# Kernel tuning notes

Hardware: AMD Instinct MI355X
Metric: run time of the kernel (lower is better)

The kernel has to match this reference:

```python
import jax, jax.numpy as jnp
import numpy as np

E, H, BLOCK = 1024, 64, 2048

def setup_inputs() -> dict:
    key = jax.random.key(0)
    kx, kk, kq, kv = jax.random.split(key, 4)
    s = 1.0 / np.sqrt(E)
    return {
        "x": jax.random.normal(kx, (16, 2048, E), dtype=jnp.float32),
        "Wk": jax.random.uniform(kk, (E, H), jnp.float32, -s, s),
        "Wq": jax.random.uniform(kq, (E, H), jnp.float32, -s, s),
        "Wv": jax.random.uniform(kv, (E, H), jnp.float32, -s, s),
    }

def reference(x, Wk, Wq, Wv):
    B, T, C = x.shape
    k = x @ Wk  # [B,T,H]
    q = x @ Wq
    v = x @ Wv
    scale = jnp.asarray(H, x.dtype) ** -0.5
    wei = jnp.einsum("bth,bsh->bts", q, k) * scale  # [B,T,T]
    causal = jnp.tril(jnp.ones((T, T), dtype=bool))
    wei = jnp.where(causal, wei, -jnp.inf)
    wei = jax.nn.softmax(wei, axis=-1)
    # dropout is identity in eval mode
    return jnp.einsum("bts,bsh->bth", wei, v)
```

## Files before the change

### kernel.cpp

```cpp
#include <hip/hip_runtime.h>


typedef __bf16 bf16x8 __attribute__((ext_vector_type(8)));
typedef __bf16 bf16x4 __attribute__((ext_vector_type(4)));
typedef float f32x4 __attribute__((ext_vector_type(4)));

constexpr int kE = 1024;
constexpr int kH = 64;
constexpr int kT = 2048;
constexpr int kB = 16;
constexpr int kM = kB * kT;
constexpr float kQScale = 0.125f * 1.44269504088896340736f;

#define MFMA16(a, b, c) __builtin_amdgcn_mfma_f32_16x16x32_bf16((a), (b), (c), 0, 0, 0)

__device__ __forceinline__ void gl_lds16(const void* g, void* l) {
    __builtin_amdgcn_global_load_lds(
        (const __attribute__((address_space(1))) void*)g,
        (__attribute__((address_space(3))) void*)l, 16, 0, 0);
}

__global__ __launch_bounds__(256)
void prep_w(const float* __restrict__ Wq, const float* __restrict__ Wk,
            const float* __restrict__ Wv, __bf16* __restrict__ WbT)
{
    __shared__ float tl[64][65];
    const int mat = blockIdx.x >> 4;
    const int k0 = (blockIdx.x & 15) * 64;
    const float* src = (mat == 0) ? Wq : (mat == 1) ? Wk : Wv;

    const int t = threadIdx.x;
    const int kr = t >> 2;
    const int cg = (t & 3) * 16;
    #pragma unroll
    for (int i = 0; i < 4; ++i) {
        float4 v = *(const float4*)&src[(size_t)(k0 + kr) * kH + cg + 4 * i];
        tl[cg + 4 * i + 0][kr] = v.x;
        tl[cg + 4 * i + 1][kr] = v.y;
        tl[cg + 4 * i + 2][kr] = v.z;
        tl[cg + 4 * i + 3][kr] = v.w;
    }
    __syncthreads();
    const int nl = t >> 2;
    const int kg = (t & 3) * 16;
    bf16x8 o0, o1;
    #pragma unroll
    for (int j = 0; j < 8; ++j) {
        o0[j] = (__bf16)tl[nl][kg + j];
        o1[j] = (__bf16)tl[nl][kg + 8 + j];
    }
    *(bf16x8*)&WbT[(size_t)(mat * 64 + nl) * kE + k0 + kg] = o0;
    *(bf16x8*)&WbT[(size_t)(mat * 64 + nl) * kE + k0 + kg + 8] = o1;
}

__global__ __launch_bounds__(256)
void qkv(const float* __restrict__ x, const __bf16* __restrict__ WbT,
         __bf16* __restrict__ qo, __bf16* __restrict__ ko, __bf16* __restrict__ vT)
{
    __shared__ __align__(16) char Ab[2][16384];
    __shared__ __align__(16) char Bb[2][24576];

    const int t = threadIdx.x;
    const int lane = t & 63;
    const int w = t >> 6;
    const int l15 = lane & 15;
    const int Q = lane >> 4;
    const int row0 = blockIdx.x * 64;

    f32x4 acc[4][3];
    #pragma unroll
    for (int mt = 0; mt < 4; ++mt)
        #pragma unroll
        for (int nt = 0; nt < 3; ++nt) acc[mt][nt] = (f32x4){0.f, 0.f, 0.f, 0.f};

    auto stage = [&](int p, int k0) {
        #pragma unroll
        for (int i = 0; i < 4; ++i) {
            const int row = (w * 4 + i) * 4 + (lane >> 4);
            const int g = (lane & 15) ^ (i * 4 + (lane >> 4));
            gl_lds16(&x[(size_t)(row0 + row) * kE + k0 + g * 4],
                     &Ab[p][(w * 4 + i) * 1024]);
        }
        #pragma unroll
        for (int i = 0; i < 6; ++i) {
            const int n = (w * 6 + i) * 8 + (lane >> 3);
            const int g = (lane & 7) ^ (lane >> 3);
            gl_lds16(&WbT[(size_t)n * kE + k0 + g * 8],
                     &Bb[p][(w * 6 + i) * 1024]);
        }
    };

    stage(0, 0);
    __syncthreads();

    for (int c = 0; c < 16; ++c) {
        const int p = c & 1;
        if (c < 15) stage(1 - p, (c + 1) * 64);

        #pragma unroll
        for (int ks = 0; ks < 2; ++ks) {
            bf16x8 a4[4];
            #pragma unroll
            for (int mt = 0; mt < 4; ++mt) {
                const int row = mt * 16 + l15;
                float4 u0 = *(const float4*)&Ab[p][row * 256 + ((ks * 8 + Q * 2 + 0) ^ l15) * 16];
                float4 u1 = *(const float4*)&Ab[p][row * 256 + ((ks * 8 + Q * 2 + 1) ^ l15) * 16];
                bf16x8 a;
                a[0] = (__bf16)u0.x; a[1] = (__bf16)u0.y;
                a[2] = (__bf16)u0.z; a[3] = (__bf16)u0.w;
                a[4] = (__bf16)u1.x; a[5] = (__bf16)u1.y;
                a[6] = (__bf16)u1.z; a[7] = (__bf16)u1.w;
                a4[mt] = a;
            }
            #pragma unroll
            for (int nt = 0; nt < 3; ++nt) {
                const int n = w * 48 + nt * 16 + l15;
                bf16x8 b = *(const bf16x8*)&Bb[p][n * 128 + (((ks * 4 + Q) ^ (l15 & 7)) * 16)];
                #pragma unroll
                for (int mt = 0; mt < 4; ++mt)
                    acc[mt][nt] = MFMA16(a4[mt], b, acc[mt][nt]);
            }
        }
        __syncthreads();
    }

    const int batch = row0 >> 11;
    const int tr0 = row0 & 2047;
    #pragma unroll
    for (int nt = 0; nt < 3; ++nt) {
        const int col0 = w * 48 + nt * 16;
        const int mat = col0 >> 6;
        const int c = (col0 & 63) + l15;
        if (mat == 2) {
            #pragma unroll
            for (int mt = 0; mt < 4; ++mt) {
                const int trow = tr0 + mt * 16 + Q * 4;
                bf16x4 pk;
                #pragma unroll
                for (int r = 0; r < 4; ++r) pk[r] = (__bf16)acc[mt][nt][r];
                *(bf16x4*)&vT[((size_t)batch * kH + c) * kT + trow] = pk;
            }
        } else {
            __bf16* dst = (mat == 0) ? qo : ko;
            const float sc_ = (mat == 0) ? kQScale : 1.0f;
            #pragma unroll
            for (int mt = 0; mt < 4; ++mt)
                #pragma unroll
                for (int r = 0; r < 4; ++r) {
                    const size_t row = row0 + mt * 16 + Q * 4 + r;
                    dst[row * kH + c] = (__bf16)(acc[mt][nt][r] * sc_);
                }
        }
    }
}

__global__ __launch_bounds__(64, 2)
void attn(const __bf16* __restrict__ qm, const __bf16* __restrict__ km,
          const __bf16* __restrict__ vT, float* __restrict__ out)
{
    __shared__ __align__(16) char Kb[8192];
    __shared__ __align__(16) char Vb[8192];
    __shared__ __align__(16) __bf16 Ps[16][72];

    const int lane = threadIdx.x;
    const int l15 = lane & 15;
    const int Q = lane >> 4;

    const int xcd  = blockIdx.x & 7;
    const int slot = blockIdx.x >> 3;
    const int batch = xcd + ((slot >> 7) << 3);
    const int s = slot & 127;
    const int q16 = ((s & 1) << 6) | ((s & 2) << 4) | ((s & 4) << 2) | (s & 8)
                  | ((s & 16) >> 2) | ((s & 32) >> 4) | ((s & 64) >> 6);
    const int qrow = q16 * 16 + l15;
    const int last = q16 >> 2;

    const __bf16* qb = qm + (size_t)batch * kT * kH;
    const __bf16* kb = km + (size_t)batch * kT * kH;
    const __bf16* vb = vT + (size_t)batch * kH * kT;

    auto stage = [&](int s0) {
        #pragma unroll
        for (int i = 0; i < 8; ++i) {
            const int n = i * 8 + (lane >> 3);
            const int g = (lane & 7) ^ (lane >> 3);
            gl_lds16(&kb[(size_t)(s0 + n) * kH + g * 8], &Kb[i * 1024]);
            gl_lds16(&vb[(size_t)n * kT + s0 + g * 8], &Vb[i * 1024]);
        }
    };

    bf16x8 aq[2];
    aq[0] = *(const bf16x8*)&qb[(size_t)qrow * kH + Q * 8];
    aq[1] = *(const bf16x8*)&qb[(size_t)qrow * kH + 32 + Q * 8];

    f32x4 O[4];
    #pragma unroll
    for (int i = 0; i < 4; ++i) O[i] = (f32x4){0.f, 0.f, 0.f, 0.f};
    float m_ = -3.0e38f, l_ = 0.f;

    stage(0);
    asm volatile("s_waitcnt vmcnt(0)" ::: "memory");

    for (int kt = 0; kt <= last; ++kt) {
        bf16x8 kf[8], vf[8];
        #pragma unroll
        for (int ks = 0; ks < 2; ++ks)
            #pragma unroll
            for (int nt = 0; nt < 4; ++nt)
                kf[ks * 4 + nt] = *(const bf16x8*)
                    &Kb[(nt * 16 + l15) * 128 + (((ks * 4 + Q) ^ (l15 & 7)) * 16)];
        #pragma unroll
        for (int ht = 0; ht < 4; ++ht)
            #pragma unroll
            for (int ss = 0; ss < 2; ++ss)
                vf[ht * 2 + ss] = *(const bf16x8*)
                    &Vb[(ht * 16 + l15) * 128 + (((ss * 4 + Q) ^ (l15 & 7)) * 16)];
        asm volatile("s_waitcnt lgkmcnt(0)" ::: "memory");

        if (kt < last) stage((kt + 1) * 64);

        f32x4 sacc[4];
        #pragma unroll
        for (int nt = 0; nt < 4; ++nt) sacc[nt] = (f32x4){0.f, 0.f, 0.f, 0.f};
        #pragma unroll
        for (int ks = 0; ks < 2; ++ks)
            #pragma unroll
            for (int nt = 0; nt < 4; ++nt)
                sacc[nt] = MFMA16(kf[ks * 4 + nt], aq[ks], sacc[nt]);

        if (kt == last) {
            const int s0 = kt * 64;
            #pragma unroll
            for (int nt = 0; nt < 4; ++nt)
                #pragma unroll
                for (int r = 0; r < 4; ++r)
                    if (s0 + nt * 16 + Q * 4 + r > qrow) sacc[nt][r] = -3.0e38f;
        }

        float mx = sacc[0][0];
        #pragma unroll
        for (int nt = 0; nt < 4; ++nt)
            #pragma unroll
            for (int r = 0; r < 4; ++r) mx = fmaxf(mx, sacc[nt][r]);
        mx = fmaxf(mx, __shfl_xor(mx, 16));
        mx = fmaxf(mx, __shfl_xor(mx, 32));
        const float mnew = fmaxf(m_, mx);
        const float alpha = __builtin_amdgcn_exp2f(m_ - mnew);
        float rs = 0.f;
        #pragma unroll
        for (int nt = 0; nt < 4; ++nt)
            #pragma unroll
            for (int r = 0; r < 4; ++r) {
                const float pv = __builtin_amdgcn_exp2f(sacc[nt][r] - mnew);
                sacc[nt][r] = pv;
                rs += pv;
            }
        rs += __shfl_xor(rs, 16);
        rs += __shfl_xor(rs, 32);
        l_ = l_ * alpha + rs;
        m_ = mnew;
        #pragma unroll
        for (int ht = 0; ht < 4; ++ht) O[ht] *= alpha;

        #pragma unroll
        for (int nt = 0; nt < 4; ++nt) {
            bf16x4 pk;
            #pragma unroll
            for (int r = 0; r < 4; ++r) pk[r] = (__bf16)sacc[nt][r];
            *(bf16x4*)&Ps[l15][nt * 16 + Q * 4] = pk;
        }
        bf16x8 pb0 = *(const bf16x8*)&Ps[l15][Q * 8];
        bf16x8 pb1 = *(const bf16x8*)&Ps[l15][32 + Q * 8];

        #pragma unroll
        for (int ht = 0; ht < 4; ++ht) {
            O[ht] = MFMA16(vf[ht * 2 + 0], pb0, O[ht]);
            O[ht] = MFMA16(vf[ht * 2 + 1], pb1, O[ht]);
        }

        asm volatile("s_waitcnt vmcnt(0)" ::: "memory");
    }

    const float inv = 1.0f / l_;
    float* orow = out + ((size_t)batch * kT + qrow) * kH;
    #pragma unroll
    for (int ht = 0; ht < 4; ++ht) {
        float4 o4;
        o4.x = O[ht][0] * inv; o4.y = O[ht][1] * inv;
        o4.z = O[ht][2] * inv; o4.w = O[ht][3] * inv;
        *(float4*)&orow[ht * 16 + Q * 4] = o4;
    }
}

extern "C" void kernel_launch(void* const* d_in, const int* in_sizes, int n_in,
                              void* d_out, int out_size, void* d_ws, size_t ws_size,
                              hipStream_t stream)
{
    (void)in_sizes; (void)n_in; (void)out_size; (void)ws_size;
    const float* x  = (const float*)d_in[0];
    const float* Wk = (const float*)d_in[1];
    const float* Wq = (const float*)d_in[2];
    const float* Wv = (const float*)d_in[3];

    __bf16* WbT  = (__bf16*)d_ws;
    __bf16* qb   = WbT + (size_t)192 * kE;
    __bf16* kbuf = qb + (size_t)kM * kH;
    __bf16* vT   = kbuf + (size_t)kM * kH;

    prep_w<<<48, 256, 0, stream>>>(Wq, Wk, Wv, WbT);
    qkv<<<kM / 64, 256, 0, stream>>>(x, WbT, qb, kbuf, vT);
    attn<<<kB * 128, 64, 0, stream>>>(qb, kbuf, vT, (float*)d_out);
}
```

Before: 262.4 us.

## Share double-buffered K/V LDS tiles across four waves per attention block

The attention kernel grows from one wave to four waves per block. The four waves handle consecutive 16-row query tiles and share K/V tiles that all four load cooperatively into double-buffered LDS, with barriers between iterations. This cuts redundant global K/V loads by about 4x and overlaps the next tile's load with compute. The block-to-work mapping now pairs a short causal tile of one batch with a long tile of another for load balance. The cost is block-wide barrier stalls. Correctness also relies on the barrier waiting for the asynchronous global-to-LDS loads, since the explicit vmcnt wait was removed.

```diff
diff --git a/kernel.cpp b/kernel.cpp
--- a/kernel.cpp
+++ b/kernel.cpp
@@ -154,38 +154,41 @@
     }
 }
 
-__global__ __launch_bounds__(64, 2)
+__global__ __launch_bounds__(256, 2)
 void attn(const __bf16* __restrict__ qm, const __bf16* __restrict__ km,
           const __bf16* __restrict__ vT, float* __restrict__ out)
 {
-    __shared__ __align__(16) char Kb[8192];
-    __shared__ __align__(16) char Vb[8192];
-    __shared__ __align__(16) __bf16 Ps[16][72];
-
-    const int lane = threadIdx.x;
+    __shared__ __align__(16) char Kb[2][8192];
+    __shared__ __align__(16) char Vb[2][8192];
+    __shared__ __align__(16) __bf16 Ps[4][16][72];
+
+    const int tid = threadIdx.x;
+    const int lane = tid & 63;
+    const int w = tid >> 6;
     const int l15 = lane & 15;
     const int Q = lane >> 4;
 
     const int xcd  = blockIdx.x & 7;
     const int slot = blockIdx.x >> 3;
-    const int batch = xcd + ((slot >> 7) << 3);
-    const int s = slot & 127;
-    const int q16 = ((s & 1) << 6) | ((s & 2) << 4) | ((s & 4) << 2) | (s & 8)
-                  | ((s & 16) >> 2) | ((s & 32) >> 4) | ((s & 64) >> 6);
+    const int batch = xcd + ((slot & 1) << 3);
+    const int tt = (slot & 1) ? (31 - (slot >> 1)) : (slot >> 1);
+    const int q16 = tt * 4 + w;
     const int qrow = q16 * 16 + l15;
-    const int last = q16 >> 2;
+    const int last = tt;
 
     const __bf16* qb = qm + (size_t)batch * kT * kH;
     const __bf16* kb = km + (size_t)batch * kT * kH;
     const __bf16* vb = vT + (size_t)batch * kH * kT;
 
-    auto stage = [&](int s0) {
-        #pragma unroll
-        for (int i = 0; i < 8; ++i) {
-            const int n = i * 8 + (lane >> 3);
+    auto stage = [&](int p, int s0) {
+        #pragma unroll
+        for (int i = 0; i < 2; ++i) {
+            const int r = w * 16 + i * 8 + (lane >> 3);
             const int g = (lane & 7) ^ (lane >> 3);
-            gl_lds16(&kb[(size_t)(s0 + n) * kH + g * 8], &Kb[i * 1024]);
-            gl_lds16(&vb[(size_t)n * kT + s0 + g * 8], &Vb[i * 1024]);
+            gl_lds16(&kb[(size_t)(s0 + r) * kH + g * 8],
+                     &Kb[p][(w * 2 + i) * 1024]);
+            gl_lds16(&vb[(size_t)r * kT + s0 + g * 8],
+                     &Vb[p][(w * 2 + i) * 1024]);
         }
     };
 
@@ -198,26 +201,28 @@
     for (int i = 0; i < 4; ++i) O[i] = (f32x4){0.f, 0.f, 0.f, 0.f};
     float m_ = -3.0e38f, l_ = 0.f;
 
-    stage(0);
-    asm volatile("s_waitcnt vmcnt(0)" ::: "memory");
+    stage(0, 0);
+    __syncthreads();
 
     for (int kt = 0; kt <= last; ++kt) {
+        const int p = kt & 1;
+
         bf16x8 kf[8], vf[8];
         #pragma unroll
         for (int ks = 0; ks < 2; ++ks)
             #pragma unroll
             for (int nt = 0; nt < 4; ++nt)
                 kf[ks * 4 + nt] = *(const bf16x8*)
-                    &Kb[(nt * 16 + l15) * 128 + (((ks * 4 + Q) ^ (l15 & 7)) * 16)];
+                    &Kb[p][(nt * 16 + l15) * 128 + (((ks * 4 + Q) ^ (l15 & 7)) * 16)];
         #pragma unroll
         for (int ht = 0; ht < 4; ++ht)
             #pragma unroll
             for (int ss = 0; ss < 2; ++ss)
                 vf[ht * 2 + ss] = *(const bf16x8*)
-                    &Vb[(ht * 16 + l15) * 128 + (((ss * 4 + Q) ^ (l15 & 7)) * 16)];
+                    &Vb[p][(ht * 16 + l15) * 128 + (((ss * 4 + Q) ^ (l15 & 7)) * 16)];
         asm volatile("s_waitcnt lgkmcnt(0)" ::: "memory");
 
-        if (kt < last) stage((kt + 1) * 64);
+        if (kt < last) stage(1 - p, (kt + 1) * 64);
 
         f32x4 sacc[4];
         #pragma unroll
@@ -267,10 +272,10 @@
             bf16x4 pk;
             #pragma unroll
             for (int r = 0; r < 4; ++r) pk[r] = (__bf16)sacc[nt][r];
-            *(bf16x4*)&Ps[l15][nt * 16 + Q * 4] = pk;
-        }
-        bf16x8 pb0 = *(const bf16x8*)&Ps[l15][Q * 8];
-        bf16x8 pb1 = *(const bf16x8*)&Ps[l15][32 + Q * 8];
+            *(bf16x4*)&Ps[w][l15][nt * 16 + Q * 4] = pk;
+        }
+        bf16x8 pb0 = *(const bf16x8*)&Ps[w][l15][Q * 8];
+        bf16x8 pb1 = *(const bf16x8*)&Ps[w][l15][32 + Q * 8];
 
         #pragma unroll
         for (int ht = 0; ht < 4; ++ht) {
@@ -278,7 +283,7 @@
             O[ht] = MFMA16(vf[ht * 2 + 1], pb1, O[ht]);
         }
 
-        asm volatile("s_waitcnt vmcnt(0)" ::: "memory");
+        __syncthreads();
     }
 
     const float inv = 1.0f / l_;
@@ -309,5 +314,5 @@
 
     prep_w<<<48, 256, 0, stream>>>(Wq, Wk, Wv, WbT);
     qkv<<<kM / 64, 256, 0, stream>>>(x, WbT, qb, kbuf, vT);
-    attn<<<kB * 128, 64, 0, stream>>>(qb, kbuf, vT, (float*)d_out);
-}
+    attn<<<512, 256, 0, stream>>>(qb, kbuf, vT, (float*)d_out);
+}
```

Measured after the change: 242.1 us. 7.8% less time.
